# Performance work log

Measured on AMD Instinct MI355X. Metric: run time of the kernel, lower is better.

## Reference

```python
import jax, jax.numpy as jnp
import numpy as np


def setup_inputs() -> dict:
    key = jax.random.key(0)
    B, S, D = 8, 4096, 4  # 8 ragged segments, 4096 points each, 4-dim coords
    coordinates = jax.random.normal(key, (B * S, D), dtype=jnp.float32)
    row_splits = jnp.arange(B + 1, dtype=jnp.int32) * S  # [0, 4096, ..., 32768]
    return {"K": 64, "coordinates": coordinates, "row_splits": row_splits}


def reference(K, coordinates, row_splits):
    # Exact per-segment kNN (squared euclidean), equivalent math to the binned
    # accelerated search. Segments are equal-sized, so reshape to [B, S, D].
    B = row_splits.shape[0] - 1
    N, D = coordinates.shape
    S = N // B
    x = coordinates.reshape(B, S, D)
    sq = jnp.sum(x * x, axis=-1)  # [B, S]
    # d2[b,i,j] = ||x_i - x_j||^2 within segment b
    d2 = sq[:, :, None] + sq[:, None, :] - 2.0 * jnp.einsum('bid,bjd->bij', x, x)
    neg_vals, idx_local = jax.lax.top_k(-d2, K)  # smallest K distances; self first (dist ~0)
    dist = jnp.maximum(-neg_vals, 0.0)  # clamp fp cancellation negatives to 0
    offsets = (jnp.arange(B, dtype=idx_local.dtype) * S)[:, None, None]
    idx = (idx_local + offsets).reshape(N, K)  # global indices
    return idx, dist.reshape(N, K)
```

## Files before the change

kernel.cpp:

```cpp
#include <hip/hip_runtime.h>
#include <math.h>

#define KNN 64

typedef unsigned long long u64;


template<int CTRL>
__device__ __forceinline__ unsigned dpp32(unsigned v) {
    return (unsigned)__builtin_amdgcn_update_dpp((int)v, (int)v, CTRL, 0xF, 0xF, false);
}

template<int J>
__device__ __forceinline__ u64 kv_exch(u64 kv, int addr32) {
    unsigned lo = (unsigned)kv, hi = (unsigned)(kv >> 32);
    unsigned rlo, rhi;
    if constexpr (J == 1) {
        rlo = dpp32<0xB1>(lo); rhi = dpp32<0xB1>(hi);
    } else if constexpr (J == 2) {
        rlo = dpp32<0x4E>(lo); rhi = dpp32<0x4E>(hi);
    } else if constexpr (J == 4) {
        rlo = dpp32<0x4E>(dpp32<0xB1>(dpp32<0x141>(lo)));
        rhi = dpp32<0x4E>(dpp32<0xB1>(dpp32<0x141>(hi)));
    } else if constexpr (J == 8) {
        rlo = dpp32<0x128>(lo); rhi = dpp32<0x128>(hi);
    } else if constexpr (J == 16) {
        rlo = (unsigned)__builtin_amdgcn_ds_swizzle((int)lo, (16 << 10) | 0x1F);
        rhi = (unsigned)__builtin_amdgcn_ds_swizzle((int)hi, (16 << 10) | 0x1F);
    } else {
        rlo = (unsigned)__builtin_amdgcn_ds_bpermute(addr32, (int)lo);
        rhi = (unsigned)__builtin_amdgcn_ds_bpermute(addr32, (int)hi);
    }
    return ((u64)rhi << 32) | (u64)rlo;
}

template<int K, int J>
__device__ __forceinline__ void ce(u64 &kv, int lane, int addr32) {
    const u64 r = kv_exch<J>(kv, addr32);
    const bool tm = ((lane & K) == 0) == ((lane & J) == 0);
    kv = ((kv < r) == tm) ? kv : r;
}

__device__ __forceinline__ void clean64(u64 &kv, int lane, int addr32) {
    ce<64,32>(kv, lane, addr32);
    ce<64,16>(kv, lane, addr32);
    ce<64, 8>(kv, lane, addr32);
    ce<64, 4>(kv, lane, addr32);
    ce<64, 2>(kv, lane, addr32);
    ce<64, 1>(kv, lane, addr32);
}

__device__ __forceinline__ u64 sort64(u64 kv, int lane, int addr32) {
    ce<2,1>(kv, lane, addr32);
    ce<4,2>(kv, lane, addr32);   ce<4,1>(kv, lane, addr32);
    ce<8,4>(kv, lane, addr32);   ce<8,2>(kv, lane, addr32);   ce<8,1>(kv, lane, addr32);
    ce<16,8>(kv, lane, addr32);  ce<16,4>(kv, lane, addr32);  ce<16,2>(kv, lane, addr32);  ce<16,1>(kv, lane, addr32);
    ce<32,16>(kv, lane, addr32); ce<32,8>(kv, lane, addr32);  ce<32,4>(kv, lane, addr32);  ce<32,2>(kv, lane, addr32);  ce<32,1>(kv, lane, addr32);
    clean64(kv, lane, addr32);
    return kv;
}

#define PAD_RAW 0x7F800000FFFFFFFFull
#define BUF_STRIDE 132

__device__ __forceinline__ void flush_merge(u64 &kv, float &worst_f,
                                            u64* __restrict__ s_buf,
                                            int lane, int addr32, int addr63) {
    const u64 raw = s_buf[lane];
    unsigned hi = (unsigned)(raw >> 32);
    hi ^= (unsigned)((int)hi >> 31) | 0x80000000u;
    u64 kvb = ((u64)hi << 32) | (unsigned)raw;
    kvb = sort64(kvb, lane, addr32);
    const unsigned rlo = (unsigned)__builtin_amdgcn_ds_bpermute(addr63, (int)(unsigned)kvb);
    const unsigned rhi = (unsigned)__builtin_amdgcn_ds_bpermute(addr63, (int)(unsigned)(kvb >> 32));
    const u64 r = ((u64)rhi << 32) | (u64)rlo;
    kv = (r < kv) ? r : kv;
    clean64(kv, lane, addr32);
    unsigned w = (unsigned)__builtin_amdgcn_readlane((int)(unsigned)(kv >> 32), 63);
    w ^= (w & 0x80000000u) ? 0x80000000u : 0xFFFFFFFFu;
    worst_f = __uint_as_float(w);
    s_buf[lane] = PAD_RAW;
}

__global__ __launch_bounds__(256) void knn_wave_kernel(
    const float4* __restrict__ coords,
    float* __restrict__ outIdx,
    float* __restrict__ outDist,
    int S, int Nq)
{
#pragma clang fp contract(off)
    extern __shared__ u64 smem_u64[];
    float* __restrict__ s_csq = (float*)smem_u64;

    const int tid   = threadIdx.x;
    const int lane  = tid & 63;
    const int wid   = tid >> 6;
    const int qbase = blockIdx.x << 2;
    const int seg_start = (qbase / S) * S;

    for (int p = tid; p < S; p += 256) {
        const float4 c = coords[seg_start + p];
        s_csq[p] = (c.x * c.x + c.z * c.z) + (c.y * c.y + c.w * c.w);
    }
    __syncthreads();

    const int q = qbase + wid;
    if (q >= Nq) return;

    u64* __restrict__ s_buf = smem_u64 + (S >> 1) + wid * BUF_STRIDE;
    const float4* __restrict__ seg = coords + seg_start;

    const float4 x = coords[q];
    const float sqx = (x.x * x.x + x.z * x.z) + (x.y * x.y + x.w * x.w);

    const int addr32 = (lane ^ 32) << 2;
    const int addr63 = (lane ^ 63) << 2;

    u64 kv = 0xFF800000FFFFFFFFull;
    float worst_f = __builtin_inff();
    s_buf[lane] = PAD_RAW;
    int bufcnt = 0;

    const int S4 = S & ~255;
    for (int c0 = 0; c0 < S4; c0 += 256) {
        float d2v[4];
        u64 mv[4];
#pragma unroll
        for (int u = 0; u < 4; ++u) {
            const int j = c0 + (u << 6) + lane;
            const float4 c = seg[j];
            const float csq = s_csq[j];
            const float dot = __builtin_fmaf(x.w, c.w,
                              __builtin_fmaf(x.z, c.z,
                              __builtin_fmaf(x.y, c.y, x.x * c.x)));
            d2v[u] = __builtin_fmaf(-2.0f, dot, sqx + csq);
            mv[u]  = __ballot(d2v[u] < worst_f);
        }
        const int p0 = __popcll(mv[0]), p1 = __popcll(mv[1]);
        const int p2 = __popcll(mv[2]), p3 = __popcll(mv[3]);
        const int cnt4 = p0 + p1 + p2 + p3;

        if (bufcnt + cnt4 <= 64) {
            const int b0 = bufcnt, b1 = b0 + p0, b2 = b1 + p1, b3 = b2 + p2;
            const int bases[4] = {b0, b1, b2, b3};
#pragma unroll
            for (int u = 0; u < 4; ++u) {
                const int pos = __builtin_amdgcn_mbcnt_hi(
                                    (unsigned)(mv[u] >> 32),
                                    __builtin_amdgcn_mbcnt_lo((unsigned)mv[u], bases[u]));
                const bool sv = d2v[u] < worst_f;
                const int slot = sv ? pos : (64 + lane);
                s_buf[slot] = ((u64)__float_as_uint(d2v[u]) << 32)
                            | (unsigned)(c0 + (u << 6) + lane);
            }
            bufcnt += cnt4;
        } else {
#pragma unroll
            for (int u = 0; u < 4; ++u) {
                bool surv = d2v[u] < worst_f;
                u64 m = mv[u];
                int cnt = __popcll(m);
                if (bufcnt + cnt > 64) {
                    flush_merge(kv, worst_f, s_buf, lane, addr32, addr63);
                    bufcnt = 0;
                    surv = d2v[u] < worst_f;
                    m = __ballot(surv);
                    cnt = __popcll(m);
                }
                if (m) {
                    const int pos = __builtin_amdgcn_mbcnt_hi(
                                        (unsigned)(m >> 32),
                                        __builtin_amdgcn_mbcnt_lo((unsigned)m, bufcnt));
                    if (surv)
                        s_buf[pos] = ((u64)__float_as_uint(d2v[u]) << 32)
                                   | (unsigned)(c0 + (u << 6) + lane);
                    bufcnt += cnt;
                }
            }
        }
    }
    for (int c0 = S4; c0 < S; c0 += 64) {
        const int j = c0 + lane;
        const float4 c = seg[j];
        const float csq = s_csq[j];
        const float dot = __builtin_fmaf(x.w, c.w,
                          __builtin_fmaf(x.z, c.z,
                          __builtin_fmaf(x.y, c.y, x.x * c.x)));
        const float d2  = __builtin_fmaf(-2.0f, dot, sqx + csq);
        bool surv = d2 < worst_f;
        u64 m = __ballot(surv);
        int cnt = __popcll(m);
        if (bufcnt + cnt > 64) {
            flush_merge(kv, worst_f, s_buf, lane, addr32, addr63);
            bufcnt = 0;
            surv = d2 < worst_f;
            m = __ballot(surv);
            cnt = __popcll(m);
        }
        if (m) {
            const int pos = __builtin_amdgcn_mbcnt_hi(
                                (unsigned)(m >> 32),
                                __builtin_amdgcn_mbcnt_lo((unsigned)m, bufcnt));
            if (surv)
                s_buf[pos] = ((u64)__float_as_uint(d2) << 32) | (unsigned)j;
            bufcnt += cnt;
        }
    }

    if (bufcnt > 0)
        flush_merge(kv, worst_f, s_buf, lane, addr32, addr63);

    const unsigned idxs = (unsigned)kv;
    unsigned bk = (unsigned)(kv >> 32);
    bk ^= ((bk & 0x80000000u) ? 0x80000000u : 0xFFFFFFFFu);
    const float d2 = __uint_as_float(bk);
    outIdx [(size_t)q * KNN + lane] = (float)(seg_start + (int)idxs);
    outDist[(size_t)q * KNN + lane] = fmaxf(d2, 0.0f);
}

extern "C" void kernel_launch(void* const* d_in, const int* in_sizes, int n_in,
                              void* d_out, int out_size, void* d_ws, size_t ws_size,
                              hipStream_t stream) {
    const float* coords = (const float*)d_in[1];
    const int N = in_sizes[1] / 4;
    const int B = in_sizes[2] - 1;
    const int S = N / B;
    (void)n_in; (void)d_ws; (void)ws_size; (void)out_size;

    float* outIdx  = (float*)d_out;
    float* outDist = outIdx + (size_t)N * KNN;

    const int blocks = (N + 3) / 4;
    const size_t smem = (size_t)S * 4 + 4 * BUF_STRIDE * 8;
    knn_wave_kernel<<<blocks, 256, smem, stream>>>((const float4*)coords,
                                                   outIdx, outDist, S, N);
}
```

Before: 206.7 us.

## Prefetch next candidate tile into registers and use branchy predicated buffer stores

Software-pipelines the candidate loop so the next 256 coordinates and squared norms are loaded into registers while the current tile is being evaluated, hiding global/LDS load latency. The compaction store now skips empty ballots and writes only surviving lanes, instead of routing non-survivors to a dump region. That removes the need for the padded 132-entry per-wave buffer, so it shrinks to 64 entries and reduces shared memory. The cost is higher register pressure from the double-buffered float4s, plus extra divergent branches in the store path.

```diff
diff --git a/kernel.cpp b/kernel.cpp
--- a/kernel.cpp
+++ b/kernel.cpp
@@ -61,7 +61,6 @@
 }
 
 #define PAD_RAW 0x7F800000FFFFFFFFull
-#define BUF_STRIDE 132
 
 __device__ __forceinline__ void flush_merge(u64 &kv, float &worst_f,
                                             u64* __restrict__ s_buf,
@@ -107,7 +106,7 @@
     const int q = qbase + wid;
     if (q >= Nq) return;
 
-    u64* __restrict__ s_buf = smem_u64 + (S >> 1) + wid * BUF_STRIDE;
+    u64* __restrict__ s_buf = smem_u64 + (S >> 1) + (wid << 6);
     const float4* __restrict__ seg = coords + seg_start;
 
     const float4 x = coords[q];
@@ -122,18 +121,38 @@
     int bufcnt = 0;
 
     const int S4 = S & ~255;
+
+    float4 pc[4]; float pcsq[4];
+#pragma unroll
+    for (int u = 0; u < 4; ++u) {
+        const int j = (u << 6) + lane;
+        pc[u]   = seg[j];
+        pcsq[u] = s_csq[j];
+    }
+
     for (int c0 = 0; c0 < S4; c0 += 256) {
+        float4 cc[4]; float ccsq[4];
+#pragma unroll
+        for (int u = 0; u < 4; ++u) { cc[u] = pc[u]; ccsq[u] = pcsq[u]; }
+
+        if (c0 + 256 < S4) {
+#pragma unroll
+            for (int u = 0; u < 4; ++u) {
+                const int j = c0 + 256 + (u << 6) + lane;
+                pc[u]   = seg[j];
+                pcsq[u] = s_csq[j];
+            }
+        }
+
         float d2v[4];
         u64 mv[4];
 #pragma unroll
         for (int u = 0; u < 4; ++u) {
-            const int j = c0 + (u << 6) + lane;
-            const float4 c = seg[j];
-            const float csq = s_csq[j];
+            const float4 c = cc[u];
             const float dot = __builtin_fmaf(x.w, c.w,
                               __builtin_fmaf(x.z, c.z,
                               __builtin_fmaf(x.y, c.y, x.x * c.x)));
-            d2v[u] = __builtin_fmaf(-2.0f, dot, sqx + csq);
+            d2v[u] = __builtin_fmaf(-2.0f, dot, sqx + ccsq[u]);
             mv[u]  = __ballot(d2v[u] < worst_f);
         }
         const int p0 = __popcll(mv[0]), p1 = __popcll(mv[1]);
@@ -141,17 +160,18 @@
         const int cnt4 = p0 + p1 + p2 + p3;
 
         if (bufcnt + cnt4 <= 64) {
-            const int b0 = bufcnt, b1 = b0 + p0, b2 = b1 + p1, b3 = b2 + p2;
-            const int bases[4] = {b0, b1, b2, b3};
+            const int bases[4] = {bufcnt, bufcnt + p0, bufcnt + p0 + p1,
+                                  bufcnt + p0 + p1 + p2};
 #pragma unroll
             for (int u = 0; u < 4; ++u) {
-                const int pos = __builtin_amdgcn_mbcnt_hi(
-                                    (unsigned)(mv[u] >> 32),
-                                    __builtin_amdgcn_mbcnt_lo((unsigned)mv[u], bases[u]));
-                const bool sv = d2v[u] < worst_f;
-                const int slot = sv ? pos : (64 + lane);
-                s_buf[slot] = ((u64)__float_as_uint(d2v[u]) << 32)
-                            | (unsigned)(c0 + (u << 6) + lane);
+                if (mv[u]) {
+                    const int pos = __builtin_amdgcn_mbcnt_hi(
+                                        (unsigned)(mv[u] >> 32),
+                                        __builtin_amdgcn_mbcnt_lo((unsigned)mv[u], bases[u]));
+                    if (d2v[u] < worst_f)
+                        s_buf[pos] = ((u64)__float_as_uint(d2v[u]) << 32)
+                                   | (unsigned)(c0 + (u << 6) + lane);
+                }
             }
             bufcnt += cnt4;
         } else {
@@ -231,7 +251,7 @@
     float* outDist = outIdx + (size_t)N * KNN;
 
     const int blocks = (N + 3) / 4;
-    const size_t smem = (size_t)S * 4 + 4 * BUF_STRIDE * 8;
+    const size_t smem = (size_t)S * 4 + 4 * 64 * 8;
     knn_wave_kernel<<<blocks, 256, smem, stream>>>((const float4*)coords,
                                                    outIdx, outDist, S, N);
 }
```

New measurement: 215.4 us. 1.04x slower.
